# Kernel tuning notes

Hardware: AMD Instinct MI355X
Metric: run time of the kernel (lower is better)

## Reference

```python
import jax, jax.numpy as jnp
import numpy as np

NEG_MASK_SCALE = -1e-09  # faithful to source (source uses -1e-09, likely intended -1e9)


def setup_inputs() -> dict:
    key0 = jax.random.key(0)
    ks = jax.random.split(key0, 7)
    B, Q, K, H = 4, 256, 1024, 128
    return {
        "query": jax.random.normal(ks[0], (B, Q, H), dtype=jnp.float32),
        "key": jax.random.normal(ks[1], (B, K, H), dtype=jnp.float32),
        "value": jax.random.normal(ks[2], (B, K, H), dtype=jnp.float32),
        "mask": jax.random.randint(ks[3], (B, Q, K), 0, 2).astype(jnp.int32),
        "Wq": jax.random.normal(ks[4], (H, H), dtype=jnp.float32) * (1.0 / np.sqrt(H)),
        "Wk": jax.random.normal(ks[5], (H, H), dtype=jnp.float32) * (1.0 / np.sqrt(H)),
        "v": jax.random.normal(ks[6], (H,), dtype=jnp.float32) * (1.0 / np.sqrt(H)),
    }


def reference(query, key, value, mask, Wq, Wk, v):
    # Projections: torch Linear computes x @ W.T
    q_proj = jnp.einsum("bqd,hd->bqh", query, Wq)  # (B, Q, H)
    k_proj = jnp.einsum("bkd,hd->bkh", key, Wk)    # (B, K, H)
    # Additive (Bahdanau) score: v . tanh(q_proj[:, :, None] + k_proj[:, None])
    feat = jnp.tanh(q_proj[:, :, None, :] + k_proj[:, None, :, :])  # (B, Q, K, H)
    score = jnp.einsum("bqkh,h->bqk", feat, v)                      # (B, Q, K)
    score = score + NEG_MASK_SCALE * (1.0 - mask.astype(score.dtype))
    attention_weights = jax.nn.softmax(score, axis=-1)              # (B, Q, K)
    context_vector = jnp.einsum("bqk,bkv->bqv", attention_weights, value)  # (B, Q, V)
    return attention_weights, context_vector
```

## Files before the change

### kernel.cpp

```cpp
#include <hip/hip_runtime.h>

#define Bb 4
#define Qn 256
#define Kn 1024
#define Hn 128
#define QT 4
#define PF 8

constexpr float SCALE = 2.88539008177792681f;

#if __has_builtin(__builtin_amdgcn_exp2f)
#define EXP2F(x) __builtin_amdgcn_exp2f(x)
#else
#define EXP2F(x) exp2f(x)
#endif
#if __has_builtin(__builtin_amdgcn_rcpf)
#define RCPF(x) __builtin_amdgcn_rcpf(x)
#else
#define RCPF(x) (1.0f / (x))
#endif

__global__ __launch_bounds__(128) void proj_kernel(const float* __restrict__ query,
                                                   const float* __restrict__ key,
                                                   const float* __restrict__ Wq,
                                                   const float* __restrict__ Wk,
                                                   float* __restrict__ eqT,
                                                   float* __restrict__ ekT) {
    __shared__ float4 xs[128];
    const int tid = threadIdx.x;
    const bool isQ = blockIdx.x < (Bb * Qn / 4);
    const int r0 = (isQ ? blockIdx.x : blockIdx.x - Bb * Qn / 4) * 4;
    const float* x = isQ ? query : key;
    const float* W = isQ ? Wq : Wk;

    xs[tid] = ((const float4*)(x + (size_t)r0 * Hn))[tid];
    __syncthreads();
    const float4* W4 = (const float4*)W + (size_t)tid * (Hn / 4);
    float acc0 = 0.f, acc1 = 0.f, acc2 = 0.f, acc3 = 0.f;
#pragma unroll 8
    for (int d = 0; d < Hn / 4; ++d) {
        float4 w = W4[d];
        float4 a0 = xs[d];
        float4 a1 = xs[32 + d];
        float4 a2 = xs[64 + d];
        float4 a3 = xs[96 + d];
        acc0 = fmaf(w.x, a0.x, fmaf(w.y, a0.y, fmaf(w.z, a0.z, fmaf(w.w, a0.w, acc0))));
        acc1 = fmaf(w.x, a1.x, fmaf(w.y, a1.y, fmaf(w.z, a1.z, fmaf(w.w, a1.w, acc1))));
        acc2 = fmaf(w.x, a2.x, fmaf(w.y, a2.y, fmaf(w.z, a2.z, fmaf(w.w, a2.w, acc2))));
        acc3 = fmaf(w.x, a3.x, fmaf(w.y, a3.y, fmaf(w.z, a3.z, fmaf(w.w, a3.w, acc3))));
    }
    float4 res = make_float4(EXP2F(acc0 * SCALE), EXP2F(acc1 * SCALE),
                             EXP2F(acc2 * SCALE), EXP2F(acc3 * SCALE));
    if (isQ) {
        const int b = r0 / Qn;
        const int q0 = r0 % Qn;
        ((float4*)eqT)[((size_t)b * Hn + tid) * (Qn / 4) + (q0 >> 2)] = res;
    } else {
        const int b = r0 / Kn;
        const int k0 = r0 % Kn;
        ((float4*)ekT)[((size_t)b * Hn + tid) * (Kn / 4) + (k0 >> 2)] = res;
    }
}

__global__ __launch_bounds__(1024) void fused_attn_kernel(const float* __restrict__ eqT,
                                                          const float* __restrict__ ekT,
                                                          const float* __restrict__ v,
                                                          const float* __restrict__ value,
                                                          float* __restrict__ attn,
                                                          float* __restrict__ ctx) {
    const int tid = threadIdx.x;
    const int q0 = blockIdx.x * QT;
    const int b = blockIdx.y;

    __shared__ __align__(16) float sc[QT][Kn];
    __shared__ float red[16][2];
    __shared__ __align__(16) float4 pl[8][QT][Hn / 4];

    const int kg = tid & 255;
    const int qu = __builtin_amdgcn_readfirstlane(tid >> 8);
    const float4* ekp = (const float4*)(ekT + (size_t)b * Hn * Kn) + kg;
    const float* eqs = eqT + (size_t)b * Hn * Qn + q0 + qu;

    float4 pf[PF];
#pragma unroll
    for (int j = 0; j < PF; ++j) pf[j] = ekp[(size_t)j * (Kn / 4)];

    float a0 = 0.f, a1 = 0.f, a2 = 0.f, a3 = 0.f;
    for (int c = 0; c < Hn / PF; ++c) {
#pragma unroll
        for (int j = 0; j < PF; ++j) {
            const int h = c * PF + j;
            const float4 kv = pf[j];
            if (c < Hn / PF - 1) pf[j] = ekp[(size_t)(h + PF) * (Kn / 4)];
            const float qe = eqs[(size_t)h * Qn];
            const float vh = v[h];
            float r;
            r = RCPF(fmaf(qe, kv.x, 1.0f)); a0 = fmaf(vh, r, a0);
            r = RCPF(fmaf(qe, kv.y, 1.0f)); a1 = fmaf(vh, r, a1);
            r = RCPF(fmaf(qe, kv.z, 1.0f)); a2 = fmaf(vh, r, a2);
            r = RCPF(fmaf(qe, kv.w, 1.0f)); a3 = fmaf(vh, r, a3);
        }
    }

    const int lane = tid & 63, wv = tid >> 6;
    float mn = fminf(fminf(a0, a1), fminf(a2, a3));
#pragma unroll
    for (int off = 32; off; off >>= 1) mn = fminf(mn, __shfl_xor(mn, off));
    if (lane == 0) red[wv][0] = mn;
    __syncthreads();
    mn = fminf(fminf(red[qu * 4][0], red[qu * 4 + 1][0]),
               fminf(red[qu * 4 + 2][0], red[qu * 4 + 3][0]));

    const float e0 = EXP2F((mn - a0) * SCALE);
    const float e1 = EXP2F((mn - a1) * SCALE);
    const float e2 = EXP2F((mn - a2) * SCALE);
    const float e3 = EXP2F((mn - a3) * SCALE);
    float s = (e0 + e1) + (e2 + e3);
#pragma unroll
    for (int off = 32; off; off >>= 1) s += __shfl_xor(s, off);
    if (lane == 0) red[wv][1] = s;
    __syncthreads();
    s = (red[qu * 4][1] + red[qu * 4 + 1][1]) +
        (red[qu * 4 + 2][1] + red[qu * 4 + 3][1]);
    const float inv = RCPF(s);

    const float4 w4 = make_float4(e0 * inv, e1 * inv, e2 * inv, e3 * inv);
    ((float4*)&sc[qu][0])[kg] = w4;
    ((float4*)(attn + ((size_t)b * Qn + q0 + qu) * Kn))[kg] = w4;
    __syncthreads();

    const int kc = tid >> 7;
    const int cq = (tid >> 5) & 3;
    const int h4 = tid & 31;
    const float4* vb = (const float4*)(value + ((size_t)b * Kn + kc * 128) * Hn) + h4;
    const float* wr = &sc[cq][kc * 128];
    float4 acc = make_float4(0.f, 0.f, 0.f, 0.f);
#pragma unroll 4
    for (int kk = 0; kk < 128; ++kk) {
        const float wgt = wr[kk];
        const float4 vv = vb[(size_t)kk * (Hn / 4)];
        acc.x = fmaf(wgt, vv.x, acc.x);
        acc.y = fmaf(wgt, vv.y, acc.y);
        acc.z = fmaf(wgt, vv.z, acc.z);
        acc.w = fmaf(wgt, vv.w, acc.w);
    }
    pl[kc][cq][h4] = acc;
    __syncthreads();
    if (tid < QT * Hn / 4) {
        const int q = tid >> 5, h = tid & 31;
        float4 r0 = pl[0][q][h], r1 = pl[1][q][h], r2 = pl[2][q][h], r3 = pl[3][q][h];
        float4 r4 = pl[4][q][h], r5 = pl[5][q][h], r6 = pl[6][q][h], r7 = pl[7][q][h];
        float4 sum;
        sum.x = ((r0.x + r1.x) + (r2.x + r3.x)) + ((r4.x + r5.x) + (r6.x + r7.x));
        sum.y = ((r0.y + r1.y) + (r2.y + r3.y)) + ((r4.y + r5.y) + (r6.y + r7.y));
        sum.z = ((r0.z + r1.z) + (r2.z + r3.z)) + ((r4.z + r5.z) + (r6.z + r7.z));
        sum.w = ((r0.w + r1.w) + (r2.w + r3.w)) + ((r4.w + r5.w) + (r6.w + r7.w));
        ((float4*)(ctx + ((size_t)b * Qn + q0 + q) * Hn))[h] = sum;
    }
}

extern "C" void kernel_launch(void* const* d_in, const int* in_sizes, int n_in,
                              void* d_out, int out_size, void* d_ws, size_t ws_size,
                              hipStream_t stream) {
    const float* query = (const float*)d_in[0];
    const float* key = (const float*)d_in[1];
    const float* value = (const float*)d_in[2];
    const float* Wq = (const float*)d_in[4];
    const float* Wk = (const float*)d_in[5];
    const float* v = (const float*)d_in[6];

    float* out = (float*)d_out;
    float* attn = out;
    float* ctx = out + (size_t)Bb * Qn * Kn;

    float* ws = (float*)d_ws;
    float* eqT = ws;
    float* ekT = ws + 131072;

    proj_kernel<<<dim3(Bb * Qn / 4 + Bb * Kn / 4), dim3(128), 0, stream>>>(
        query, key, Wq, Wk, eqT, ekT);
    fused_attn_kernel<<<dim3(Qn / QT, Bb), dim3(1024), 0, stream>>>(
        eqT, ekT, v, value, attn, ctx);
}
```

Measured before the change: 118.1 us.

## Split fused attention into per-query score/softmax and separate context kernels

Replaces the fused kernel, which handled four queries per block with float4 key reuse, with a score+softmax kernel that runs one query per block and one key per thread, and a separate context kernel that reads the attention weights back from global memory. The query projection is stored row-major so each block reads one contiguous query row. This adds blocks and simplifies indexing, but drops the register reuse of each key load across four keys, adds a kernel launch, and round-trips the attention matrix through global memory.

```diff
diff --git a/kernel.cpp b/kernel.cpp
--- a/kernel.cpp
+++ b/kernel.cpp
@@ -4,8 +4,6 @@
 #define Qn 256
 #define Kn 1024
 #define Hn 128
-#define QT 4
-#define PF 8
 
 constexpr float SCALE = 2.88539008177792681f;
 
@@ -24,7 +22,7 @@
                                                    const float* __restrict__ key,
                                                    const float* __restrict__ Wq,
                                                    const float* __restrict__ Wk,
-                                                   float* __restrict__ eqT,
+                                                   float* __restrict__ eq,
                                                    float* __restrict__ ekT) {
     __shared__ float4 xs[128];
     const int tid = threadIdx.x;
@@ -49,91 +47,80 @@
         acc2 = fmaf(w.x, a2.x, fmaf(w.y, a2.y, fmaf(w.z, a2.z, fmaf(w.w, a2.w, acc2))));
         acc3 = fmaf(w.x, a3.x, fmaf(w.y, a3.y, fmaf(w.z, a3.z, fmaf(w.w, a3.w, acc3))));
     }
-    float4 res = make_float4(EXP2F(acc0 * SCALE), EXP2F(acc1 * SCALE),
-                             EXP2F(acc2 * SCALE), EXP2F(acc3 * SCALE));
     if (isQ) {
-        const int b = r0 / Qn;
-        const int q0 = r0 % Qn;
-        ((float4*)eqT)[((size_t)b * Hn + tid) * (Qn / 4) + (q0 >> 2)] = res;
+        eq[(size_t)(r0 + 0) * Hn + tid] = EXP2F(acc0 * SCALE);
+        eq[(size_t)(r0 + 1) * Hn + tid] = EXP2F(acc1 * SCALE);
+        eq[(size_t)(r0 + 2) * Hn + tid] = EXP2F(acc2 * SCALE);
+        eq[(size_t)(r0 + 3) * Hn + tid] = EXP2F(acc3 * SCALE);
     } else {
         const int b = r0 / Kn;
         const int k0 = r0 % Kn;
+        float4 res = make_float4(EXP2F(acc0 * SCALE), EXP2F(acc1 * SCALE),
+                                 EXP2F(acc2 * SCALE), EXP2F(acc3 * SCALE));
         ((float4*)ekT)[((size_t)b * Hn + tid) * (Kn / 4) + (k0 >> 2)] = res;
     }
 }
 
-__global__ __launch_bounds__(1024) void fused_attn_kernel(const float* __restrict__ eqT,
-                                                          const float* __restrict__ ekT,
-                                                          const float* __restrict__ v,
-                                                          const float* __restrict__ value,
-                                                          float* __restrict__ attn,
-                                                          float* __restrict__ ctx) {
-    const int tid = threadIdx.x;
-    const int q0 = blockIdx.x * QT;
+__global__ __launch_bounds__(1024) void score_softmax_kernel(const float* __restrict__ eq,
+                                                             const float* __restrict__ ekT,
+                                                             const float* __restrict__ v,
+                                                             float* __restrict__ attn) {
+    const int k = threadIdx.x;
+    const int q = blockIdx.x;
     const int b = blockIdx.y;
 
-    __shared__ __align__(16) float sc[QT][Kn];
     __shared__ float red[16][2];
-    __shared__ __align__(16) float4 pl[8][QT][Hn / 4];
 
-    const int kg = tid & 255;
-    const int qu = __builtin_amdgcn_readfirstlane(tid >> 8);
-    const float4* ekp = (const float4*)(ekT + (size_t)b * Hn * Kn) + kg;
-    const float* eqs = eqT + (size_t)b * Hn * Qn + q0 + qu;
+    const float* eqrow = eq + ((size_t)b * Qn + q) * Hn;
+    const float* ekb = ekT + (size_t)b * Hn * Kn + k;
 
-    float4 pf[PF];
-#pragma unroll
-    for (int j = 0; j < PF; ++j) pf[j] = ekp[(size_t)j * (Kn / 4)];
-
-    float a0 = 0.f, a1 = 0.f, a2 = 0.f, a3 = 0.f;
-    for (int c = 0; c < Hn / PF; ++c) {
-#pragma unroll
-        for (int j = 0; j < PF; ++j) {
-            const int h = c * PF + j;
-            const float4 kv = pf[j];
-            if (c < Hn / PF - 1) pf[j] = ekp[(size_t)(h + PF) * (Kn / 4)];
-            const float qe = eqs[(size_t)h * Qn];
-            const float vh = v[h];
-            float r;
-            r = RCPF(fmaf(qe, kv.x, 1.0f)); a0 = fmaf(vh, r, a0);
-            r = RCPF(fmaf(qe, kv.y, 1.0f)); a1 = fmaf(vh, r, a1);
-            r = RCPF(fmaf(qe, kv.z, 1.0f)); a2 = fmaf(vh, r, a2);
-            r = RCPF(fmaf(qe, kv.w, 1.0f)); a3 = fmaf(vh, r, a3);
-        }
+    float a = 0.f;
+#pragma unroll 16
+    for (int h = 0; h < Hn; ++h) {
+        const float qe = eqrow[h];
+        const float vh = v[h];
+        const float kv = ekb[(size_t)h * Kn];
+        const float r = RCPF(fmaf(qe, kv, 1.0f));
+        a = fmaf(vh, r, a);
     }
 
-    const int lane = tid & 63, wv = tid >> 6;
-    float mn = fminf(fminf(a0, a1), fminf(a2, a3));
+    const int lane = k & 63, wv = k >> 6;
+    float mn = a;
 #pragma unroll
     for (int off = 32; off; off >>= 1) mn = fminf(mn, __shfl_xor(mn, off));
     if (lane == 0) red[wv][0] = mn;
     __syncthreads();
-    mn = fminf(fminf(red[qu * 4][0], red[qu * 4 + 1][0]),
-               fminf(red[qu * 4 + 2][0], red[qu * 4 + 3][0]));
+    mn = red[0][0];
+#pragma unroll
+    for (int w = 1; w < 16; ++w) mn = fminf(mn, red[w][0]);
 
-    const float e0 = EXP2F((mn - a0) * SCALE);
-    const float e1 = EXP2F((mn - a1) * SCALE);
-    const float e2 = EXP2F((mn - a2) * SCALE);
-    const float e3 = EXP2F((mn - a3) * SCALE);
-    float s = (e0 + e1) + (e2 + e3);
+    const float e = EXP2F((mn - a) * SCALE);
+    float s = e;
 #pragma unroll
     for (int off = 32; off; off >>= 1) s += __shfl_xor(s, off);
     if (lane == 0) red[wv][1] = s;
     __syncthreads();
-    s = (red[qu * 4][1] + red[qu * 4 + 1][1]) +
-        (red[qu * 4 + 2][1] + red[qu * 4 + 3][1]);
-    const float inv = RCPF(s);
+    s = red[0][1];
+#pragma unroll
+    for (int w = 1; w < 16; ++w) s += red[w][1];
 
-    const float4 w4 = make_float4(e0 * inv, e1 * inv, e2 * inv, e3 * inv);
-    ((float4*)&sc[qu][0])[kg] = w4;
-    ((float4*)(attn + ((size_t)b * Qn + q0 + qu) * Kn))[kg] = w4;
-    __syncthreads();
+    attn[((size_t)b * Qn + q) * Kn + k] = e * RCPF(s);
+}
+
+__global__ __launch_bounds__(1024) void ctx_kernel(const float* __restrict__ attn,
+                                                   const float* __restrict__ value,
+                                                   float* __restrict__ ctx) {
+    const int tid = threadIdx.x;
+    const int q0 = blockIdx.x * 4;
+    const int b = blockIdx.y;
+
+    __shared__ __align__(16) float4 pl[8][4][Hn / 4];
 
     const int kc = tid >> 7;
     const int cq = (tid >> 5) & 3;
     const int h4 = tid & 31;
     const float4* vb = (const float4*)(value + ((size_t)b * Kn + kc * 128) * Hn) + h4;
-    const float* wr = &sc[cq][kc * 128];
+    const float* wr = attn + ((size_t)b * Qn + q0 + cq) * Kn + kc * 128;
     float4 acc = make_float4(0.f, 0.f, 0.f, 0.f);
 #pragma unroll 4
     for (int kk = 0; kk < 128; ++kk) {
@@ -146,7 +133,7 @@
     }
     pl[kc][cq][h4] = acc;
     __syncthreads();
-    if (tid < QT * Hn / 4) {
+    if (tid < 128) {
         const int q = tid >> 5, h = tid & 31;
         float4 r0 = pl[0][q][h], r1 = pl[1][q][h], r2 = pl[2][q][h], r3 = pl[3][q][h];
         float4 r4 = pl[4][q][h], r5 = pl[5][q][h], r6 = pl[6][q][h], r7 = pl[7][q][h];
@@ -174,11 +161,13 @@
     float* ctx = out + (size_t)Bb * Qn * Kn;
 
     float* ws = (float*)d_ws;
-    float* eqT = ws;
+    float* eq = ws;
     float* ekT = ws + 131072;
 
     proj_kernel<<<dim3(Bb * Qn / 4 + Bb * Kn / 4), dim3(128), 0, stream>>>(
-        query, key, Wq, Wk, eqT, ekT);
-    fused_attn_kernel<<<dim3(Qn / QT, Bb), dim3(1024), 0, stream>>>(
-        eqT, ekT, v, value, attn, ctx);
+        query, key, Wq, Wk, eq, ekT);
+    score_softmax_kernel<<<dim3(Qn, Bb), dim3(1024), 0, stream>>>(
+        eq, ekT, v, attn);
+    ctx_kernel<<<dim3(Qn / 4, Bb), dim3(1024), 0, stream>>>(
+        attn, value, ctx);
 }
```

New measurement: 130.1 us. 1.1x slower.
